# Kernel tuning notes

Measured on AMD Instinct MI355X. Metric: run time of the kernel, lower is better.

Reference implementation:

```python
import jax, jax.numpy as jnp
import numpy as np


def setup_inputs() -> dict:
    key = jax.random.key(0)
    k1, k2, k3, k4 = jax.random.split(key, 4)
    L, d, n_tokens = 4096, 2048, 4096
    x = jax.random.normal(k1, (L, d), dtype=jnp.float32)
    Wq_w = jax.random.normal(k2, (d, d), dtype=jnp.float32) * (1.0 / np.sqrt(d))
    Pk = jax.random.normal(k3, (1, n_tokens, d), dtype=jnp.float32)
    Pv = jax.random.normal(k4, (1, n_tokens, d), dtype=jnp.float32)
    return {"x": x, "Wq_w": Wq_w, "Pk": Pk, "Pv": Pv, "sliding_window_size": 1024}


def reference(x, Wq_w, Pk, Pv, sliding_window_size):
    # x: (L, d); Pk/Pv: (1, n_tokens, d). Single-head cross attention to a
    # fixed parameter token bank with a bidirectional sliding-window mask
    # |q_idx - kv_idx| < sliding_window_size (flex_attention semantics,
    # default scale = 1/sqrt(d)).
    L, d = x.shape
    n_tokens = Pk.shape[1]
    scale = 1.0 / np.sqrt(d).astype(np.float32)

    q = x @ Wq_w.T                                    # (L, d)
    scores = jnp.einsum('ld,td->lt', q, Pk[0]) * scale  # (L, n_tokens)

    q_idx = jnp.arange(L)[:, None]
    kv_idx = jnp.arange(n_tokens)[None, :]
    mask = jnp.abs(q_idx - kv_idx) < sliding_window_size  # (L, n_tokens)

    neg_inf = jnp.asarray(jnp.finfo(scores.dtype).min, scores.dtype)
    probs = jax.nn.softmax(jnp.where(mask, scores, neg_inf), axis=-1)
    y = jnp.einsum('lt,td->ld', probs, Pv[0])         # (L, d)
    return y[None, :, :]                              # (1, L, d) after squeeze(1)
```

## Files before the change

kernel.cpp:

```cpp
#include <hip/hip_runtime.h>


using bf16x8 = __attribute__((ext_vector_type(8))) short;
using f32x4  = __attribute__((ext_vector_type(4))) float;

#define LDIM 4096
#define TDIM 4096
#define DDIM 2048

static __device__ __forceinline__ unsigned short f2bf(float f) {
  union { float f; unsigned u; } c; c.f = f;
  unsigned r = c.u + 0x7FFFu + ((c.u >> 16) & 1u);
  return (unsigned short)(r >> 16);
}
static __device__ __forceinline__ unsigned pack2(float a, float b) {
  return (unsigned)f2bf(a) | ((unsigned)f2bf(b) << 16);
}
static __device__ __forceinline__ void gload16(const void* g, void* l) {
  __builtin_amdgcn_global_load_lds((const __attribute__((address_space(1))) void*)g,
                                   (__attribute__((address_space(3))) void*)l, 16, 0, 0);
}

__global__ __launch_bounds__(256) void k_prep(const float* __restrict__ x,
                                              const float* __restrict__ Wq,
                                              const float* __restrict__ Pk,
                                              const float* __restrict__ Pv,
                                              unsigned short* __restrict__ xb,
                                              unsigned short* __restrict__ wb,
                                              unsigned short* __restrict__ kb,
                                              unsigned short* __restrict__ vt,
                                              float* __restrict__ rowsum) {
  const int tid = threadIdx.x;
  const int b = blockIdx.x;
  if (b < 10240) {
    const float* in; unsigned short* out; size_t i;
    if (b < 4096)      { in = x;  out = xb; i = (size_t)b * 256 + tid; }
    else if (b < 6144) { in = Wq; out = wb; i = (size_t)(b - 4096) * 256 + tid; }
    else               { in = Pk; out = kb; i = (size_t)(b - 6144) * 256 + tid; }
    const float4* p = (const float4*)(in + i * 8);
    float4 a = p[0], c = p[1];
    uint4 o = { pack2(a.x, a.y), pack2(a.z, a.w), pack2(c.x, c.y), pack2(c.z, c.w) };
    *(uint4*)(out + i * 8) = o;
    return;
  }
  if (b == 12288) {
    for (int k = tid; k < LDIM; k += 256) rowsum[k] = 0.f;
    return;
  }
  __shared__ unsigned short tile[64][72];
  const int b2 = b - 10240;
  const int t0 = (b2 & 63) * 64, j0 = (b2 >> 6) * 64;
  const int r = tid >> 4, c4 = (tid & 15) * 4;
#pragma unroll
  for (int rr = 0; rr < 64; rr += 16) {
    float4 v = *(const float4*)(Pv + (size_t)(t0 + r + rr) * DDIM + j0 + c4);
    tile[c4 + 0][r + rr] = f2bf(v.x);
    tile[c4 + 1][r + rr] = f2bf(v.y);
    tile[c4 + 2][r + rr] = f2bf(v.z);
    tile[c4 + 3][r + rr] = f2bf(v.w);
  }
  __syncthreads();
  const int jr = tid >> 3, tc = (tid & 7) * 8;
#pragma unroll
  for (int jj = 0; jj < 64; jj += 32)
    *(uint4*)(vt + (size_t)(j0 + jr + jj) * TDIM + t0 + tc) =
        *(const uint4*)&tile[jr + jj][tc];
}

static __device__ __forceinline__ void gemm_loop(const unsigned short* __restrict__ A,
                                                 const unsigned short* __restrict__ B,
                                                 int m0, int n0, long lda, long ldb,
                                                 int kbeg, int kend,
                                                 unsigned short* As, unsigned short* Bs,
                                                 f32x4 (&acc)[4][2]) {
  const int tid = threadIdx.x;
  const int wave = tid >> 6, lane = tid & 63;
  const int quad = lane >> 4, l16 = lane & 15;
  const int wm = wave >> 2, wn = wave & 3;
  const int srow = wave * 16 + (lane >> 3);
  const int scb  = (lane & 7) ^ (lane >> 3);

  const unsigned short* gA = A + (long)(m0 + srow) * lda + scb * 8;
  const unsigned short* gB = B + (long)(n0 + srow) * ldb + scb * 8;
  unsigned short* lA = As + wave * 1024;
  unsigned short* lB = Bs + wave * 1024;

  const int sw = (l16 & 7) * 8;

  for (int k0 = kbeg; k0 < kend; k0 += 64) {
    gload16(gA + k0,           lA);
    gload16(gA + k0 + 8 * lda, lA + 512);
    gload16(gB + k0,           lB);
    gload16(gB + k0 + 8 * ldb, lB + 512);
    __syncthreads();
    bf16x8 af[4][2], bfr[2][2];
#pragma unroll
    for (int i = 0; i < 4; i++)
#pragma unroll
      for (int h = 0; h < 2; h++)
        af[i][h] = *(const bf16x8*)&As[(wm * 64 + i * 16 + l16) * 64 +
                                       (((h * 4 + quad) * 8) ^ sw)];
#pragma unroll
    for (int j = 0; j < 2; j++)
#pragma unroll
      for (int h = 0; h < 2; h++)
        bfr[j][h] = *(const bf16x8*)&Bs[(wn * 32 + j * 16 + l16) * 64 +
                                        (((h * 4 + quad) * 8) ^ sw)];
#pragma unroll
    for (int h = 0; h < 2; h++)
#pragma unroll
      for (int i = 0; i < 4; i++)
#pragma unroll
        for (int j = 0; j < 2; j++)
          acc[i][j] = __builtin_amdgcn_mfma_f32_16x16x32_bf16(af[i][h], bfr[j][h],
                                                              acc[i][j], 0, 0, 0);
    __syncthreads();
  }
}

__global__ __launch_bounds__(512) void k1_qgemm(const unsigned short* __restrict__ X,
                                                const unsigned short* __restrict__ W,
                                                unsigned short* __restrict__ q) {
  __shared__ __align__(16) unsigned short As[128 * 64];
  __shared__ __align__(16) unsigned short Bs[128 * 64];
  f32x4 acc[4][2] = {};
  const int m0 = blockIdx.y * 128, n0 = blockIdx.x * 128;
  gemm_loop(X, W, m0, n0, DDIM, DDIM, 0, DDIM, As, Bs, acc);
  const int tid = threadIdx.x;
  const int wave = tid >> 6, lane = tid & 63;
  const int quad = lane >> 4, l16 = lane & 15, wm = wave >> 2, wn = wave & 3;
#pragma unroll
  for (int i = 0; i < 4; i++)
#pragma unroll
    for (int j = 0; j < 2; j++)
#pragma unroll
      for (int r = 0; r < 4; r++) {
        int row = m0 + wm * 64 + i * 16 + quad * 4 + r;
        int col = n0 + wn * 32 + j * 16 + l16;
        q[(long)row * DDIM + col] = f2bf(acc[i][j][r]);
      }
}

__global__ __launch_bounds__(512) void k2_qk(const unsigned short* __restrict__ Q,
                                             const unsigned short* __restrict__ Kb,
                                             unsigned short* __restrict__ P,
                                             float* __restrict__ rowsum,
                                             const int* __restrict__ wptr) {
  const int w = *wptr;
  const int l0 = blockIdx.y * 128, t0 = blockIdx.x * 128;
  int lo = l0 - w + 1; if (lo < 0) lo = 0;
  int hi = l0 + 127 + w - 1; if (hi > TDIM - 1) hi = TDIM - 1;
  if ((int)blockIdx.x < (lo >> 7) || (int)blockIdx.x > (hi >> 7)) return;
  __shared__ __align__(16) unsigned short As[128 * 64];
  __shared__ __align__(16) unsigned short Bs[128 * 64];
  f32x4 acc[4][2] = {};
  gemm_loop(Q, Kb, l0, t0, DDIM, DDIM, 0, DDIM, As, Bs, acc);
  const float scale = 0.022097086912079608f;
  const int tid = threadIdx.x;
  const int wave = tid >> 6, lane = tid & 63;
  const int quad = lane >> 4, l16 = lane & 15, wm = wave >> 2, wn = wave & 3;
#pragma unroll
  for (int i = 0; i < 4; i++) {
    float rs[4] = {0.f, 0.f, 0.f, 0.f};
#pragma unroll
    for (int j = 0; j < 2; j++)
#pragma unroll
      for (int r = 0; r < 4; r++) {
        int l = l0 + wm * 64 + i * 16 + quad * 4 + r;
        int t = t0 + wn * 32 + j * 16 + l16;
        int dlt = l - t; dlt = dlt < 0 ? -dlt : dlt;
        float e = 0.f;
        if (dlt < w) e = __expf(acc[i][j][r] * scale);
        unsigned short bv = f2bf(e);
        P[(long)l * TDIM + t] = bv;
        rs[r] += __uint_as_float((unsigned)bv << 16);
      }
#pragma unroll
    for (int r = 0; r < 4; ++r) {
      float s = rs[r];
      s += __shfl_xor(s, 1);
      s += __shfl_xor(s, 2);
      s += __shfl_xor(s, 4);
      s += __shfl_xor(s, 8);
      if (l16 == 0) atomicAdd(&rowsum[l0 + wm * 64 + i * 16 + quad * 4 + r], s);
    }
  }
}

__global__ __launch_bounds__(512) void k3_pv(const unsigned short* __restrict__ P,
                                             const unsigned short* __restrict__ Vt,
                                             const float* __restrict__ rowsum,
                                             float* __restrict__ Y,
                                             const int* __restrict__ wptr) {
  const int w = *wptr;
  const int l0 = blockIdx.y * 128, j0 = blockIdx.x * 128;
  int lo = l0 - w + 1; if (lo < 0) lo = 0;
  int hi = l0 + 127 + w - 1; if (hi > TDIM - 1) hi = TDIM - 1;
  const int kb = (lo >> 7) * 128, ke = ((hi >> 7) + 1) * 128;
  __shared__ __align__(16) unsigned short As[128 * 64];
  __shared__ __align__(16) unsigned short Bs[128 * 64];
  f32x4 acc[4][2] = {};
  gemm_loop(P, Vt, l0, j0, TDIM, TDIM, kb, ke, As, Bs, acc);
  const int tid = threadIdx.x;
  const int wave = tid >> 6, lane = tid & 63;
  const int quad = lane >> 4, l16 = lane & 15, wm = wave >> 2, wn = wave & 3;
#pragma unroll
  for (int i = 0; i < 4; i++)
#pragma unroll
    for (int r = 0; r < 4; r++) {
      const int l = l0 + wm * 64 + i * 16 + quad * 4 + r;
      const float inv = 1.0f / rowsum[l];
#pragma unroll
      for (int j = 0; j < 2; j++)
        Y[(long)l * DDIM + j0 + wn * 32 + j * 16 + l16] = acc[i][j][r] * inv;
    }
}

extern "C" void kernel_launch(void* const* d_in, const int* in_sizes, int n_in,
                              void* d_out, int out_size, void* d_ws, size_t ws_size,
                              hipStream_t stream) {
  const float* x  = (const float*)d_in[0];
  const float* Wq = (const float*)d_in[1];
  const float* Pk = (const float*)d_in[2];
  const float* Pv = (const float*)d_in[3];
  const int* wptr = (const int*)d_in[4];
  float* Y = (float*)d_out;

  unsigned short* base = (unsigned short*)d_ws;
  unsigned short* Pm = base;
  unsigned short* xb = base;
  unsigned short* wb = base + (size_t)LDIM * DDIM;
  unsigned short* kb = base + (size_t)TDIM * TDIM;
  unsigned short* vt = kb + (size_t)TDIM * DDIM;
  unsigned short* qb = vt + (size_t)DDIM * TDIM;
  float* rowsum = (float*)(qb + (size_t)LDIM * DDIM);

  k_prep<<<12289, 256, 0, stream>>>(x, Wq, Pk, Pv, xb, wb, kb, vt, rowsum);
  k1_qgemm<<<dim3(DDIM / 128, LDIM / 128), 512, 0, stream>>>(xb, wb, qb);
  k2_qk<<<dim3(TDIM / 128, LDIM / 128), 512, 0, stream>>>(qb, kb, Pm, rowsum, wptr);
  k3_pv<<<dim3(DDIM / 128, LDIM / 128), 512, 0, stream>>>(Pm, vt, rowsum, Y, wptr);
}
```

Before: 278.9 us.

## Double-buffer LDS tiles in GEMM loop and swizzle block order for L2 reuse

The shared GEMM loop now uses two LDS buffers, issuing global-to-LDS loads for the next K tile while MFMAs run on the current one. This hides memory latency that the single-buffer loop left exposed behind each barrier. All three GEMM kernels also remap the flat block index with an XCD-style swizzle so that neighbouring tiles share L2. LDS use doubles to 64KB per block, which may lower occupancy, and the loop steps by 128 so K ranges must be multiples of 128.

Result: slower. 306.1 us (+9.7%).

```diff
diff --git a/kernel.cpp b/kernel.cpp
--- a/kernel.cpp
+++ b/kernel.cpp
@@ -7,6 +7,8 @@
 #define LDIM 4096
 #define TDIM 4096
 #define DDIM 2048
+
+#define HBUF 8192
 
 static __device__ __forceinline__ unsigned short f2bf(float f) {
   union { float f; unsigned u; } c; c.f = f;
@@ -87,44 +89,60 @@
 
   const int sw = (l16 & 7) * 8;
 
-  for (int k0 = kbeg; k0 < kend; k0 += 64) {
-    gload16(gA + k0,           lA);
-    gload16(gA + k0 + 8 * lda, lA + 512);
-    gload16(gB + k0,           lB);
-    gload16(gB + k0 + 8 * ldb, lB + 512);
+#define STAGE(k0, bo) do {                                    \
+    gload16(gA + (k0),           lA + (bo));                  \
+    gload16(gA + (k0) + 8 * lda, lA + (bo) + 512);            \
+    gload16(gB + (k0),           lB + (bo));                  \
+    gload16(gB + (k0) + 8 * ldb, lB + (bo) + 512); } while (0)
+
+#define COMPUTE(bo) do {                                                          \
+    bf16x8 af[4][2], bfr[2][2];                                                   \
+    _Pragma("unroll")                                                             \
+    for (int i = 0; i < 4; i++)                                                   \
+      _Pragma("unroll")                                                           \
+      for (int h = 0; h < 2; h++)                                                 \
+        af[i][h] = *(const bf16x8*)&As[(bo) + (wm * 64 + i * 16 + l16) * 64 +     \
+                                       (((h * 4 + quad) * 8) ^ sw)];              \
+    _Pragma("unroll")                                                             \
+    for (int j = 0; j < 2; j++)                                                   \
+      _Pragma("unroll")                                                           \
+      for (int h = 0; h < 2; h++)                                                 \
+        bfr[j][h] = *(const bf16x8*)&Bs[(bo) + (wn * 32 + j * 16 + l16) * 64 +    \
+                                        (((h * 4 + quad) * 8) ^ sw)];             \
+    _Pragma("unroll")                                                             \
+    for (int h = 0; h < 2; h++)                                                   \
+      _Pragma("unroll")                                                           \
+      for (int i = 0; i < 4; i++)                                                 \
+        _Pragma("unroll")                                                         \
+        for (int j = 0; j < 2; j++)                                               \
+          acc[i][j] = __builtin_amdgcn_mfma_f32_16x16x32_bf16(af[i][h], bfr[j][h],\
+                                                              acc[i][j], 0, 0, 0);\
+  } while (0)
+
+  STAGE(kbeg, 0);
+  __syncthreads();
+  for (int k0 = kbeg; k0 < kend; k0 += 128) {
+    STAGE(k0 + 64, HBUF);
+    COMPUTE(0);
     __syncthreads();
-    bf16x8 af[4][2], bfr[2][2];
-#pragma unroll
-    for (int i = 0; i < 4; i++)
-#pragma unroll
-      for (int h = 0; h < 2; h++)
-        af[i][h] = *(const bf16x8*)&As[(wm * 64 + i * 16 + l16) * 64 +
-                                       (((h * 4 + quad) * 8) ^ sw)];
-#pragma unroll
-    for (int j = 0; j < 2; j++)
-#pragma unroll
-      for (int h = 0; h < 2; h++)
-        bfr[j][h] = *(const bf16x8*)&Bs[(wn * 32 + j * 16 + l16) * 64 +
-                                        (((h * 4 + quad) * 8) ^ sw)];
-#pragma unroll
-    for (int h = 0; h < 2; h++)
-#pragma unroll
-      for (int i = 0; i < 4; i++)
-#pragma unroll
-        for (int j = 0; j < 2; j++)
-          acc[i][j] = __builtin_amdgcn_mfma_f32_16x16x32_bf16(af[i][h], bfr[j][h],
-                                                              acc[i][j], 0, 0, 0);
+    if (k0 + 128 < kend) STAGE(k0 + 128, 0);
+    COMPUTE(HBUF);
     __syncthreads();
   }
+#undef STAGE
+#undef COMPUTE
 }
 
 __global__ __launch_bounds__(512) void k1_qgemm(const unsigned short* __restrict__ X,
                                                 const unsigned short* __restrict__ W,
                                                 unsigned short* __restrict__ q) {
-  __shared__ __align__(16) unsigned short As[128 * 64];
-  __shared__ __align__(16) unsigned short Bs[128 * 64];
+  __shared__ __align__(16) unsigned short As[2 * HBUF];
+  __shared__ __align__(16) unsigned short Bs[2 * HBUF];
+  const unsigned flat = blockIdx.y * 16 + blockIdx.x;
+  const unsigned swz = (flat & 7) * 64 + (flat >> 3);
+  const int bx = swz & 15, by = swz >> 4;
   f32x4 acc[4][2] = {};
-  const int m0 = blockIdx.y * 128, n0 = blockIdx.x * 128;
+  const int m0 = by * 128, n0 = bx * 128;
   gemm_loop(X, W, m0, n0, DDIM, DDIM, 0, DDIM, As, Bs, acc);
   const int tid = threadIdx.x;
   const int wave = tid >> 6, lane = tid & 63;
@@ -146,13 +164,16 @@
                                              unsigned short* __restrict__ P,
                                              float* __restrict__ rowsum,
                                              const int* __restrict__ wptr) {
+  const unsigned flat = blockIdx.y * 32 + blockIdx.x;
+  const unsigned swz = (flat & 7) * 128 + (flat >> 3);
+  const int bx = swz & 31, by = swz >> 5;
   const int w = *wptr;
-  const int l0 = blockIdx.y * 128, t0 = blockIdx.x * 128;
+  const int l0 = by * 128, t0 = bx * 128;
   int lo = l0 - w + 1; if (lo < 0) lo = 0;
   int hi = l0 + 127 + w - 1; if (hi > TDIM - 1) hi = TDIM - 1;
-  if ((int)blockIdx.x < (lo >> 7) || (int)blockIdx.x > (hi >> 7)) return;
-  __shared__ __align__(16) unsigned short As[128 * 64];
-  __shared__ __align__(16) unsigned short Bs[128 * 64];
+  if (bx < (lo >> 7) || bx > (hi >> 7)) return;
+  __shared__ __align__(16) unsigned short As[2 * HBUF];
+  __shared__ __align__(16) unsigned short Bs[2 * HBUF];
   f32x4 acc[4][2] = {};
   gemm_loop(Q, Kb, l0, t0, DDIM, DDIM, 0, DDIM, As, Bs, acc);
   const float scale = 0.022097086912079608f;
@@ -192,13 +213,16 @@
                                              const float* __restrict__ rowsum,
                                              float* __restrict__ Y,
                                              const int* __restrict__ wptr) {
+  const unsigned flat = blockIdx.y * 16 + blockIdx.x;
+  const unsigned swz = (flat & 7) * 64 + (flat >> 3);
+  const int bx = swz & 15, by = swz >> 4;
   const int w = *wptr;
-  const int l0 = blockIdx.y * 128, j0 = blockIdx.x * 128;
+  const int l0 = by * 128, j0 = bx * 128;
   int lo = l0 - w + 1; if (lo < 0) lo = 0;
   int hi = l0 + 127 + w - 1; if (hi > TDIM - 1) hi = TDIM - 1;
   const int kb = (lo >> 7) * 128, ke = ((hi >> 7) + 1) * 128;
-  __shared__ __align__(16) unsigned short As[128 * 64];
-  __shared__ __align__(16) unsigned short Bs[128 * 64];
+  __shared__ __align__(16) unsigned short As[2 * HBUF];
+  __shared__ __align__(16) unsigned short Bs[2 * HBUF];
   f32x4 acc[4][2] = {};
   gemm_loop(P, Vt, l0, j0, TDIM, TDIM, kb, ke, As, Bs, acc);
   const int tid = threadIdx.x;
```

## Fold Pk/Pv bf16 conversion and rowsum zeroing into the Q-projection GEMM kernel

Applied to the files above, without the earlier changes.

The prep kernel now converts only x and Wq. The Pk conversion, the Pv convert-and-transpose, and the rowsum zeroing move into extra blocks of the Q GEMM launch, which now uses a flat 1D grid. The memory-bound conversion work can then run on compute units alongside the compute-bound GEMM blocks instead of in a serial pre-pass. In exchange, the GEMM kernel's LDS and register footprint applies to the conversion blocks too, and GEMM tiles may be slowed by bandwidth contention.

Measured after the change: 270.7 us. -3.0%, faster.

```diff
diff --git a/kernel.cpp b/kernel.cpp
--- a/kernel.cpp
+++ b/kernel.cpp
@@ -23,56 +23,25 @@
 
 __global__ __launch_bounds__(256) void k_prep(const float* __restrict__ x,
                                               const float* __restrict__ Wq,
-                                              const float* __restrict__ Pk,
-                                              const float* __restrict__ Pv,
                                               unsigned short* __restrict__ xb,
-                                              unsigned short* __restrict__ wb,
-                                              unsigned short* __restrict__ kb,
-                                              unsigned short* __restrict__ vt,
-                                              float* __restrict__ rowsum) {
+                                              unsigned short* __restrict__ wb) {
   const int tid = threadIdx.x;
   const int b = blockIdx.x;
-  if (b < 10240) {
-    const float* in; unsigned short* out; size_t i;
-    if (b < 4096)      { in = x;  out = xb; i = (size_t)b * 256 + tid; }
-    else if (b < 6144) { in = Wq; out = wb; i = (size_t)(b - 4096) * 256 + tid; }
-    else               { in = Pk; out = kb; i = (size_t)(b - 6144) * 256 + tid; }
-    const float4* p = (const float4*)(in + i * 8);
-    float4 a = p[0], c = p[1];
-    uint4 o = { pack2(a.x, a.y), pack2(a.z, a.w), pack2(c.x, c.y), pack2(c.z, c.w) };
-    *(uint4*)(out + i * 8) = o;
-    return;
-  }
-  if (b == 12288) {
-    for (int k = tid; k < LDIM; k += 256) rowsum[k] = 0.f;
-    return;
-  }
-  __shared__ unsigned short tile[64][72];
-  const int b2 = b - 10240;
-  const int t0 = (b2 & 63) * 64, j0 = (b2 >> 6) * 64;
-  const int r = tid >> 4, c4 = (tid & 15) * 4;
-#pragma unroll
-  for (int rr = 0; rr < 64; rr += 16) {
-    float4 v = *(const float4*)(Pv + (size_t)(t0 + r + rr) * DDIM + j0 + c4);
-    tile[c4 + 0][r + rr] = f2bf(v.x);
-    tile[c4 + 1][r + rr] = f2bf(v.y);
-    tile[c4 + 2][r + rr] = f2bf(v.z);
-    tile[c4 + 3][r + rr] = f2bf(v.w);
-  }
-  __syncthreads();
-  const int jr = tid >> 3, tc = (tid & 7) * 8;
-#pragma unroll
-  for (int jj = 0; jj < 64; jj += 32)
-    *(uint4*)(vt + (size_t)(j0 + jr + jj) * TDIM + t0 + tc) =
-        *(const uint4*)&tile[jr + jj][tc];
-}
-
-static __device__ __forceinline__ void gemm_loop(const unsigned short* __restrict__ A,
-                                                 const unsigned short* __restrict__ B,
-                                                 int m0, int n0, long lda, long ldb,
-                                                 int kbeg, int kend,
-                                                 unsigned short* As, unsigned short* Bs,
-                                                 f32x4 (&acc)[4][2]) {
+  const float* in; unsigned short* out; size_t i;
+  if (b < 4096) { in = x;  out = xb; i = (size_t)b * 256 + tid; }
+  else          { in = Wq; out = wb; i = (size_t)(b - 4096) * 256 + tid; }
+  const float4* p = (const float4*)(in + i * 8);
+  float4 a = p[0], c = p[1];
+  uint4 o = { pack2(a.x, a.y), pack2(a.z, a.w), pack2(c.x, c.y), pack2(c.z, c.w) };
+  *(uint4*)(out + i * 8) = o;
+}
+
+static __device__ __forceinline__ void gemm_loop8(const unsigned short* __restrict__ A,
+                                                  const unsigned short* __restrict__ B,
+                                                  int m0, int n0, long lda, long ldb,
+                                                  int kbeg, int kend,
+                                                  unsigned short* As, unsigned short* Bs,
+                                                  f32x4 (&acc)[4][2]) {
   const int tid = threadIdx.x;
   const int wave = tid >> 6, lane = tid & 63;
   const int quad = lane >> 4, l16 = lane & 15;
@@ -118,27 +87,64 @@
   }
 }
 
-__global__ __launch_bounds__(512) void k1_qgemm(const unsigned short* __restrict__ X,
+__global__ __launch_bounds__(512) void k1_fused(const unsigned short* __restrict__ X,
                                                 const unsigned short* __restrict__ W,
-                                                unsigned short* __restrict__ q) {
+                                                const float* __restrict__ Pk,
+                                                const float* __restrict__ Pv,
+                                                unsigned short* __restrict__ q,
+                                                unsigned short* __restrict__ kb,
+                                                unsigned short* __restrict__ vt,
+                                                float* __restrict__ rowsum) {
   __shared__ __align__(16) unsigned short As[128 * 64];
   __shared__ __align__(16) unsigned short Bs[128 * 64];
-  f32x4 acc[4][2] = {};
-  const int m0 = blockIdx.y * 128, n0 = blockIdx.x * 128;
-  gemm_loop(X, W, m0, n0, DDIM, DDIM, 0, DDIM, As, Bs, acc);
-  const int tid = threadIdx.x;
-  const int wave = tid >> 6, lane = tid & 63;
-  const int quad = lane >> 4, l16 = lane & 15, wm = wave >> 2, wn = wave & 3;
-#pragma unroll
-  for (int i = 0; i < 4; i++)
-#pragma unroll
-    for (int j = 0; j < 2; j++)
-#pragma unroll
-      for (int r = 0; r < 4; r++) {
-        int row = m0 + wm * 64 + i * 16 + quad * 4 + r;
-        int col = n0 + wn * 32 + j * 16 + l16;
-        q[(long)row * DDIM + col] = f2bf(acc[i][j][r]);
-      }
+  const int tid = threadIdx.x;
+  const int b = blockIdx.x;
+
+  if (b < 512) {
+    f32x4 acc[4][2] = {};
+    const int m0 = (b >> 4) * 128, n0 = (b & 15) * 128;
+    gemm_loop8(X, W, m0, n0, DDIM, DDIM, 0, DDIM, As, Bs, acc);
+    const int wave = tid >> 6, lane = tid & 63;
+    const int quad = lane >> 4, l16 = lane & 15, wm = wave >> 2, wn = wave & 3;
+#pragma unroll
+    for (int i = 0; i < 4; i++)
+#pragma unroll
+      for (int j = 0; j < 2; j++)
+#pragma unroll
+        for (int r = 0; r < 4; r++) {
+          int row = m0 + wm * 64 + i * 16 + quad * 4 + r;
+          int col = n0 + wn * 32 + j * 16 + l16;
+          q[(long)row * DDIM + col] = f2bf(acc[i][j][r]);
+        }
+    return;
+  }
+  if (b < 2560) {
+    size_t i = (size_t)(b - 512) * 512 + tid;
+    const float4* p = (const float4*)(Pk + i * 8);
+    float4 a = p[0], c = p[1];
+    uint4 o = { pack2(a.x, a.y), pack2(a.z, a.w), pack2(c.x, c.y), pack2(c.z, c.w) };
+    *(uint4*)(kb + i * 8) = o;
+    return;
+  }
+  if (b == 4608) {
+    for (int k = tid; k < LDIM; k += 512) rowsum[k] = 0.f;
+    return;
+  }
+  unsigned short (*tile)[72] = (unsigned short (*)[72])As;
+  const int b2 = b - 2560;
+  const int t0 = (b2 & 63) * 64, j0 = (b2 >> 6) * 64;
+  const int r = tid >> 4, c4 = (tid & 15) * 4;
+#pragma unroll
+  for (int rr = 0; rr < 64; rr += 32) {
+    float4 v = *(const float4*)(Pv + (size_t)(t0 + r + rr) * DDIM + j0 + c4);
+    tile[c4 + 0][r + rr] = f2bf(v.x);
+    tile[c4 + 1][r + rr] = f2bf(v.y);
+    tile[c4 + 2][r + rr] = f2bf(v.z);
+    tile[c4 + 3][r + rr] = f2bf(v.w);
+  }
+  __syncthreads();
+  const int jr = tid >> 3, tc = (tid & 7) * 8;
+  *(uint4*)(vt + (size_t)(j0 + jr) * TDIM + t0 + tc) = *(const uint4*)&tile[jr][tc];
 }
 
 __global__ __launch_bounds__(512) void k2_qk(const unsigned short* __restrict__ Q,
@@ -154,7 +160,7 @@
   __shared__ __align__(16) unsigned short As[128 * 64];
   __shared__ __align__(16) unsigned short Bs[128 * 64];
   f32x4 acc[4][2] = {};
-  gemm_loop(Q, Kb, l0, t0, DDIM, DDIM, 0, DDIM, As, Bs, acc);
+  gemm_loop8(Q, Kb, l0, t0, DDIM, DDIM, 0, DDIM, As, Bs, acc);
   const float scale = 0.022097086912079608f;
   const int tid = threadIdx.x;
   const int wave = tid >> 6, lane = tid & 63;
@@ -200,7 +206,7 @@
   __shared__ __align__(16) unsigned short As[128 * 64];
   __shared__ __align__(16) unsigned short Bs[128 * 64];
   f32x4 acc[4][2] = {};
-  gemm_loop(P, Vt, l0, j0, TDIM, TDIM, kb, ke, As, Bs, acc);
+  gemm_loop8(P, Vt, l0, j0, TDIM, TDIM, kb, ke, As, Bs, acc);
   const int tid = threadIdx.x;
   const int wave = tid >> 6, lane = tid & 63;
   const int quad = lane >> 4, l16 = lane & 15, wm = wave >> 2, wn = wave & 3;
@@ -235,8 +241,8 @@
   unsigned short* qb = vt + (size_t)DDIM * TDIM;
   float* rowsum = (float*)(qb + (size_t)LDIM * DDIM);
 
-  k_prep<<<12289, 256, 0, stream>>>(x, Wq, Pk, Pv, xb, wb, kb, vt, rowsum);
-  k1_qgemm<<<dim3(DDIM / 128, LDIM / 128), 512, 0, stream>>>(xb, wb, qb);
+  k_prep<<<6144, 256, 0, stream>>>(x, Wq, xb, wb);
+  k1_fused<<<4609, 512, 0, stream>>>(xb, wb, Pk, Pv, qb, kb, vt, rowsum);
   k2_qk<<<dim3(TDIM / 128, LDIM / 128), 512, 0, stream>>>(qb, kb, Pm, rowsum, wptr);
   k3_pv<<<dim3(DDIM / 128, LDIM / 128), 512, 0, stream>>>(Pm, vt, rowsum, Y, wptr);
 }
```
